# Performance work log

Measured on AMD Instinct MI355X. Metric: run time of the kernel, lower is better.

Reference implementation:

```python
import jax, jax.numpy as jnp
import numpy as np


def setup_inputs() -> dict:
    key = jax.random.key(0)
    kx, ky = jax.random.split(key)
    N, M, D = 16384, 16384, 512
    x = jax.random.normal(kx, (N, D), dtype=jnp.float32)
    y = jax.random.normal(ky, (M, D), dtype=jnp.float32)
    return {"x": x, "y": y, "device": 0}


def reference(x, y, device):
    # torch.cdist(x, y, p=2): pairwise Euclidean distances [N, M]
    # matching torch's large-matrix cdist path), clamped for numerical safety.
    x_sq = jnp.sum(x * x, axis=1, keepdims=True)          # [N, 1]
    y_sq = jnp.sum(y * y, axis=1)                          # [M]
    sq_dists = x_sq + y_sq[None, :] - 2.0 * (x @ y.T)      # [N, M]
    dists = jnp.sqrt(jnp.maximum(sq_dists, 0.0))
    # min over centers (dim=1), then argmax over candidates (dim=0)
    min_dists = jnp.min(dists, axis=1)                     # [N]
    max_id = jnp.argmax(min_dists)
    max_val = min_dists[max_id]
    return max_val, max_id
```

## Files before the change

### kernel.cpp

```cpp
#include <hip/hip_runtime.h>
#include <hip/hip_fp8.h>
#include <math.h>

#define N_ROWS 16384
#define M_ROWS 16384
#define DIM    512
#define JS     8
#define KCAND  256
#define DELTA  0.40f

typedef __attribute__((ext_vector_type(8))) int   int8v;
typedef __attribute__((ext_vector_type(4))) int   int4v;
typedef __attribute__((ext_vector_type(4))) float floatx4;

__global__ __launch_bounds__(256) void convert_kernel(const float* __restrict__ x, const float* __restrict__ y,
                                                      unsigned char* __restrict__ xh8, unsigned char* __restrict__ yh8,
                                                      float* __restrict__ x_sq, float* __restrict__ y_sq,
                                                      unsigned int* __restrict__ gmax_bits,
                                                      unsigned int* __restrict__ cnt, int* __restrict__ cand) {
    if (blockIdx.x == 0) {
        if (threadIdx.x < KCAND) cand[threadIdx.x] = 0;
        if (threadIdx.x == 0) { *gmax_bits = 0u; *cnt = 0u; }
    }
    int wave = threadIdx.x >> 6, lane = threadIdx.x & 63;
    int row = blockIdx.x * 4 + wave;
    const float* src; unsigned char* dst8; float* dsq; int r;
    if (row < N_ROWS) { r = row;          src = x; dst8 = xh8; dsq = x_sq; }
    else              { r = row - N_ROWS; src = y; dst8 = yh8; dsq = y_sq; }
    const float4* s4 = (const float4*)(src + (size_t)r * DIM);
    float4 a = s4[lane * 2];
    float4 b = s4[lane * 2 + 1];
    float v[8] = {a.x, a.y, a.z, a.w, b.x, b.y, b.z, b.w};
    union { unsigned char b[8]; uint2 u2; } pk;
    float s = 0.f;
    #pragma unroll
    for (int i = 0; i < 8; ++i) {
        s += v[i] * v[i];
        __hip_fp8_e4m3 q(v[i]);
        pk.b[i] = (unsigned char)q.__x;
    }
    *(uint2*)(dst8 + (size_t)r * DIM + lane * 8) = pk.u2;
    #pragma unroll
    for (int off = 32; off > 0; off >>= 1) s += __shfl_down(s, off, 64);
    if (lane == 0) dsq[r] = s;
}

__global__ __launch_bounds__(512, 2) void pass1_kernel(const unsigned char* __restrict__ xh8,
                                                       const unsigned char* __restrict__ yh8,
                                                       const float* __restrict__ y_sq,
                                                       float* __restrict__ part) {
    __shared__ __align__(16) unsigned char Bs[4][16384];
    __shared__ __align__(16) float ysq_s[M_ROWS / JS];
    __shared__ float red[4][128];

    const int t = threadIdx.x;
    const int w = t >> 6, lane = t & 63;
    const int col = lane & 15, q = lane >> 4;
    const int h = w >> 2, c = w & 3;

    const int bid = blockIdx.x;
    const int wg = (bid & 7) * 128 + (bid >> 3);
    const int js = wg >> 7;
    const int i0 = (wg & 127) * 128;
    const int jbase = js * (M_ROWS / JS);

    {
        const float4* ys4 = (const float4*)(y_sq + jbase);
        *(float4*)&ysq_s[t * 4] = ys4[t];
    }

    {
        const unsigned char* gs = xh8 + (size_t)i0 * DIM;
        unsigned char* ls = (unsigned char*)Bs;
        #pragma unroll
        for (int it = 0; it < 8; ++it) {
            int s  = it * 512 + t;
            int r  = s >> 5;
            int u  = s & 31;
            int kq = u >> 3;
            int cl = (u & 7) ^ (r & 7);
            __builtin_amdgcn_global_load_lds(
                (const __attribute__((address_space(1))) void*)(gs + r * 512 + kq * 128 + cl * 16),
                (__attribute__((address_space(3))) void*)(ls + it * 8192 + w * 1024),
                16, 0, 0);
        }
    }
    __syncthreads();

    int8v afr[4][4];
    {
        const unsigned char* ab = (const unsigned char*)Bs;
        #pragma unroll
        for (int mt = 0; mt < 4; ++mt) {
            int rr = h * 64 + mt * 16 + col;
            #pragma unroll
            for (int kc = 0; kc < 4; ++kc) {
                int base = rr * 512 + kc * 128 + (((q << 1) ^ (rr & 7)) << 4);
                int4v a0 = *(const int4v*)(ab + base);
                int4v a1 = *(const int4v*)(ab + (base ^ 16));
                int8v f;
                f[0] = a0[0]; f[1] = a0[1]; f[2] = a0[2]; f[3] = a0[3];
                f[4] = a1[0]; f[5] = a1[1]; f[6] = a1[2]; f[7] = a1[3];
                afr[mt][kc] = f;
            }
        }
    }
    __syncthreads();

    int spo[2];
    {
        #pragma unroll
        for (int i = 0; i < 2; ++i) {
            int s  = i * 512 + t;
            int g  = s >> 7, u = s & 127;
            int jl = (g << 4) + (u & 15);
            int c2 = (u >> 4) ^ (u & 7);
            spo[i] = jl * DIM + c2 * 16;
        }
    }
    const unsigned char* tb = yh8 + (size_t)jbase * DIM;
    const int Klane = col * 16 + (((q << 1) ^ (col & 7)) << 8);

    float minv[16];
    #pragma unroll
    for (int i = 0; i < 16; ++i) minv[i] = __builtin_inff();

#define STAGE(BUF, TOFF)                                                                     \
    { _Pragma("unroll")                                                                      \
      for (int i_ = 0; i_ < 2; ++i_) {                                                       \
          __builtin_amdgcn_global_load_lds(                                                  \
              (const __attribute__((address_space(1))) void*)(tb + spo[i_] + (TOFF)),        \
              (__attribute__((address_space(3))) void*)(&Bs[BUF][i_ * 8192 + w * 1024]),     \
              16, 0, 0);                                                                     \
      } }

    STAGE(0, 0)
    STAGE(1, 128)

    for (int jt = 0; jt < 16; ++jt) {
        floatx4 acc[4][2];
        #pragma unroll
        for (int mt = 0; mt < 4; ++mt) {
            acc[mt][0] = (floatx4){0.f, 0.f, 0.f, 0.f};
            acc[mt][1] = (floatx4){0.f, 0.f, 0.f, 0.f};
        }
        #pragma unroll
        for (int kc = 0; kc < 4; ++kc) {
            const int jtp  = (jt + (kc >> 1)) & 15;
            const int toff = jtp * (128 * DIM) + (((kc + 2) & 3) << 7);
            STAGE((kc + 2) & 3, toff)
            asm volatile("s_waitcnt vmcnt(4)" ::: "memory");
            __builtin_amdgcn_s_barrier();
            asm volatile("" ::: "memory");
            #pragma unroll
            for (int nt = 0; nt < 2; ++nt) {
                const unsigned char* gb = &Bs[kc][(c * 2 + nt) * 2048];
                int4v lo = *(const int4v*)(gb + Klane);
                int4v hi = *(const int4v*)(gb + (Klane ^ 256));
                int8v b;
                b[0] = lo[0]; b[1] = lo[1]; b[2] = lo[2]; b[3] = lo[3];
                b[4] = hi[0]; b[5] = hi[1]; b[6] = hi[2]; b[7] = hi[3];
                __builtin_amdgcn_s_setprio(1);
                #pragma unroll
                for (int mt = 0; mt < 4; ++mt)
                    acc[mt][nt] = __builtin_amdgcn_mfma_scale_f32_16x16x128_f8f6f4(
                        afr[mt][kc], b, acc[mt][nt], 0, 0, 0, 127, 0, 127);
                __builtin_amdgcn_s_setprio(0);
            }
        }
        #pragma unroll
        for (int nt = 0; nt < 2; ++nt) {
            float qv = ysq_s[jt * 128 + c * 32 + nt * 16 + col];
            #pragma unroll
            for (int mt = 0; mt < 4; ++mt)
                #pragma unroll
                for (int r = 0; r < 4; ++r)
                    minv[mt * 4 + r] = fminf(minv[mt * 4 + r], qv - 2.f * acc[mt][nt][r]);
        }
    }
#undef STAGE

    #pragma unroll
    for (int i = 0; i < 16; ++i) {
        float v = minv[i];
        v = fminf(v, __shfl_xor(v, 1, 64));
        v = fminf(v, __shfl_xor(v, 2, 64));
        v = fminf(v, __shfl_xor(v, 4, 64));
        v = fminf(v, __shfl_xor(v, 8, 64));
        minv[i] = v;
    }
    if (col == 0) {
        #pragma unroll
        for (int mt = 0; mt < 4; ++mt)
            #pragma unroll
            for (int r = 0; r < 4; ++r)
                red[c][h * 64 + mt * 16 + q * 4 + r] = minv[mt * 4 + r];
    }
    __syncthreads();
    if (t < 128)
        part[(size_t)(i0 + t) * JS + js] =
            fminf(fminf(red[0][t], red[1][t]), fminf(red[2][t], red[3][t]));
}

__global__ __launch_bounds__(1024) void maxred_kernel(const float* __restrict__ part,
                                                      const float* __restrict__ x_sq,
                                                      float* __restrict__ aval,
                                                      unsigned int* __restrict__ gmax_bits) {
    __shared__ float sm[1024];
    int t = threadIdx.x;
    int row = blockIdx.x * 1024 + t;
    float m = part[(size_t)row * JS];
    #pragma unroll
    for (int c = 1; c < JS; ++c) m = fminf(m, part[(size_t)row * JS + c]);
    float v = sqrtf(fmaxf(x_sq[row] + m, 0.f));
    aval[row] = v;
    sm[t] = v;
    __syncthreads();
    for (int s = 512; s > 0; s >>= 1) {
        if (t < s) sm[t] = fmaxf(sm[t], sm[t + s]);
        __syncthreads();
    }
    if (t == 0) atomicMax(gmax_bits, __float_as_uint(sm[0]));
}

__global__ __launch_bounds__(1024) void select_kernel(const float* __restrict__ aval,
                                                      const unsigned int* __restrict__ gmax_bits,
                                                      unsigned int* __restrict__ cnt,
                                                      int* __restrict__ cand) {
    int row = blockIdx.x * 1024 + threadIdx.x;
    float gmax = __uint_as_float(*gmax_bits);
    if (aval[row] >= gmax - DELTA) {
        unsigned s = atomicAdd(cnt, 1u);
        if (s < KCAND) cand[s] = row;
    }
}

#define TIr 64
#define LDA 68
#define LDB 132
__global__ __launch_bounds__(256) void rescore_kernel(const float* __restrict__ x, const float* __restrict__ y,
                                                      const float* __restrict__ y_sq,
                                                      const int* __restrict__ cand,
                                                      const unsigned int* __restrict__ cnt,
                                                      float* __restrict__ part2) {
    __shared__ __align__(16) float As[32 * LDA];
    __shared__ __align__(16) float Bs[32 * LDB];
    __shared__ float red[TIr][17];

    int t = threadIdx.x;
    int tx = t & 15, ty = t >> 4;
    int i0 = blockIdx.x * TIr;
    int j0 = blockIdx.y * 128;

    if ((unsigned)i0 >= *cnt) return;

    float acc[4][8];
    #pragma unroll
    for (int c = 0; c < 4; ++c)
        #pragma unroll
        for (int d = 0; d < 8; ++d) acc[c][d] = 0.f;

    int srow = t >> 3;
    int skq = (t & 7) * 4;
    int grow0 = cand[i0 + srow];
    int grow1 = cand[i0 + 32 + srow];

    for (int kc = 0; kc < DIM; kc += 32) {
        {
            float4 v = *(const float4*)(x + (size_t)grow0 * DIM + kc + skq);
            As[(skq + 0) * LDA + srow] = v.x;
            As[(skq + 1) * LDA + srow] = v.y;
            As[(skq + 2) * LDA + srow] = v.z;
            As[(skq + 3) * LDA + srow] = v.w;
            v = *(const float4*)(x + (size_t)grow1 * DIM + kc + skq);
            As[(skq + 0) * LDA + 32 + srow] = v.x;
            As[(skq + 1) * LDA + 32 + srow] = v.y;
            As[(skq + 2) * LDA + 32 + srow] = v.z;
            As[(skq + 3) * LDA + 32 + srow] = v.w;
        }
        #pragma unroll
        for (int it = 0; it < 4; ++it) {
            int row = it * 32 + srow;
            float4 v = *(const float4*)(y + (size_t)(j0 + row) * DIM + kc + skq);
            Bs[(skq + 0) * LDB + row] = v.x;
            Bs[(skq + 1) * LDB + row] = v.y;
            Bs[(skq + 2) * LDB + row] = v.z;
            Bs[(skq + 3) * LDB + row] = v.w;
        }
        __syncthreads();
        #pragma unroll 8
        for (int k = 0; k < 32; ++k) {
            float4 a  = *(const float4*)&As[k * LDA + ty * 4];
            float4 b0 = *(const float4*)&Bs[k * LDB + tx * 8];
            float4 b1 = *(const float4*)&Bs[k * LDB + tx * 8 + 4];
            float av[4] = {a.x, a.y, a.z, a.w};
            float bv[8] = {b0.x, b0.y, b0.z, b0.w, b1.x, b1.y, b1.z, b1.w};
            #pragma unroll
            for (int c = 0; c < 4; ++c)
                #pragma unroll
                for (int d = 0; d < 8; ++d)
                    acc[c][d] = fmaf(av[c], bv[d], acc[c][d]);
        }
        __syncthreads();
    }

    float4 q0 = *(const float4*)(y_sq + j0 + tx * 8);
    float4 q1 = *(const float4*)(y_sq + j0 + tx * 8 + 4);
    float qv[8] = {q0.x, q0.y, q0.z, q0.w, q1.x, q1.y, q1.z, q1.w};
    float mv[4] = {__builtin_inff(), __builtin_inff(), __builtin_inff(), __builtin_inff()};
    #pragma unroll
    for (int c = 0; c < 4; ++c)
        #pragma unroll
        for (int d = 0; d < 8; ++d)
            mv[c] = fminf(mv[c], qv[d] - 2.f * acc[c][d]);
    #pragma unroll
    for (int c = 0; c < 4; ++c) red[ty * 4 + c][tx] = mv[c];
    __syncthreads();
    if (t < TIr) {
        float m = red[t][0];
        #pragma unroll
        for (int xx = 1; xx < 16; ++xx) m = fminf(m, red[t][xx]);
        part2[(size_t)(i0 + t) * 128 + blockIdx.y] = m;
    }
}

__global__ __launch_bounds__(256) void final2_kernel(const float* __restrict__ part2,
                                                     const float* __restrict__ x_sq,
                                                     const int* __restrict__ cand,
                                                     const unsigned int* __restrict__ cnt,
                                                     float* __restrict__ out) {
    __shared__ float sv[256];
    __shared__ int si[256];
    int t = threadIdx.x;
    const float4* p4 = (const float4*)(part2 + (size_t)t * 128);
    float m = __builtin_inff();
    for (int c = 0; c < 32; ++c) {
        float4 v = p4[c];
        m = fminf(m, fminf(fminf(v.x, v.y), fminf(v.z, v.w)));
    }
    unsigned n = *cnt;
    if (n > KCAND) n = KCAND;
    int row = cand[t];
    float v = (t < (int)n) ? sqrtf(fmaxf(x_sq[row] + m, 0.f)) : -__builtin_inff();
    sv[t] = v; si[t] = row;
    __syncthreads();
    for (int s = 128; s > 0; s >>= 1) {
        if (t < s) {
            float v2 = sv[t + s]; int i2 = si[t + s];
            if (v2 > sv[t] || (v2 == sv[t] && i2 < si[t])) { sv[t] = v2; si[t] = i2; }
        }
        __syncthreads();
    }
    if (t == 0) { out[0] = sv[0]; out[1] = (float)si[0]; }
}

extern "C" void kernel_launch(void* const* d_in, const int* in_sizes, int n_in,
                              void* d_out, int out_size, void* d_ws, size_t ws_size,
                              hipStream_t stream) {
    const float* x = (const float*)d_in[0];
    const float* y = (const float*)d_in[1];
    float* out = (float*)d_out;

    char* w = (char*)d_ws;
    unsigned char* xh8 = (unsigned char*)w;
    unsigned char* yh8 = (unsigned char*)(w + (size_t)8388608);
    float* x_sq = (float*)(w + (size_t)16777216);
    float* y_sq = x_sq + N_ROWS;
    float* part = y_sq + M_ROWS;
    float* aval = part + (size_t)N_ROWS * JS;
    float* part2 = aval + N_ROWS;
    int* cand = (int*)(part2 + KCAND * 128);
    unsigned int* gmax_bits = (unsigned int*)(cand + KCAND);
    unsigned int* cnt = gmax_bits + 1;

    convert_kernel<<<(N_ROWS + M_ROWS) / 4, 256, 0, stream>>>(x, y, xh8, yh8, x_sq, y_sq, gmax_bits, cnt, cand);
    pass1_kernel<<<1024, 512, 0, stream>>>(xh8, yh8, y_sq, part);
    maxred_kernel<<<N_ROWS / 1024, 1024, 0, stream>>>(part, x_sq, aval, gmax_bits);
    select_kernel<<<N_ROWS / 1024, 1024, 0, stream>>>(aval, gmax_bits, cnt, cand);
    dim3 g2(KCAND / TIr, M_ROWS / 128);
    rescore_kernel<<<g2, 256, 0, stream>>>(x, y, y_sq, cand, cnt, part2);
    final2_kernel<<<1, 256, 0, stream>>>(part2, x_sq, cand, cnt, out);
}
```

Before: 285.4 us.

## Give each wave a private LDS ring for B tiles and drop per-step barriers

Shrinks the pass1 block from 8 waves to 4. Each wave now computes a 64x64 output sub-tile (4 N-tiles instead of 2) and streams its own slice of the Y tile into a private LDS region, so the per-k-step workgroup barrier can be removed. Waves then wait only on their own outstanding global-to-LDS loads. LDS use grows to about 128KB per block, which limits occupancy to one block of 4 waves per CU and raises accumulator register pressure.

```diff
diff --git a/kernel.cpp b/kernel.cpp
--- a/kernel.cpp
+++ b/kernel.cpp
@@ -45,18 +45,18 @@
     if (lane == 0) dsq[r] = s;
 }
 
-__global__ __launch_bounds__(512, 2) void pass1_kernel(const unsigned char* __restrict__ xh8,
+__global__ __launch_bounds__(256, 1) void pass1_kernel(const unsigned char* __restrict__ xh8,
                                                        const unsigned char* __restrict__ yh8,
                                                        const float* __restrict__ y_sq,
                                                        float* __restrict__ part) {
-    __shared__ __align__(16) unsigned char Bs[4][16384];
+    __shared__ __align__(16) unsigned char Bs[4][32768];
     __shared__ __align__(16) float ysq_s[M_ROWS / JS];
-    __shared__ float red[4][128];
+    __shared__ float red[2][128];
 
     const int t = threadIdx.x;
     const int w = t >> 6, lane = t & 63;
     const int col = lane & 15, q = lane >> 4;
-    const int h = w >> 2, c = w & 3;
+    const int h = w >> 1, c = w & 1;
 
     const int bid = blockIdx.x;
     const int wg = (bid & 7) * 128 + (bid >> 3);
@@ -66,22 +66,25 @@
 
     {
         const float4* ys4 = (const float4*)(y_sq + jbase);
-        *(float4*)&ysq_s[t * 4] = ys4[t];
+        float4 v0 = ys4[t * 2];
+        float4 v1 = ys4[t * 2 + 1];
+        *(float4*)&ysq_s[t * 8]     = v0;
+        *(float4*)&ysq_s[t * 8 + 4] = v1;
     }
 
     {
         const unsigned char* gs = xh8 + (size_t)i0 * DIM;
         unsigned char* ls = (unsigned char*)Bs;
         #pragma unroll
-        for (int it = 0; it < 8; ++it) {
-            int s  = it * 512 + t;
+        for (int it = 0; it < 16; ++it) {
+            int s  = it * 256 + t;
             int r  = s >> 5;
             int u  = s & 31;
             int kq = u >> 3;
             int cl = (u & 7) ^ (r & 7);
             __builtin_amdgcn_global_load_lds(
                 (const __attribute__((address_space(1))) void*)(gs + r * 512 + kq * 128 + cl * 16),
-                (__attribute__((address_space(3))) void*)(ls + it * 8192 + w * 1024),
+                (__attribute__((address_space(3))) void*)(ls + it * 4096 + w * 1024),
                 16, 0, 0);
         }
     }
@@ -107,18 +110,19 @@
     }
     __syncthreads();
 
-    int spo[2];
+    int spo[8];
     {
         #pragma unroll
-        for (int i = 0; i < 2; ++i) {
-            int s  = i * 512 + t;
+        for (int i = 0; i < 8; ++i) {
+            int s  = i * 64 + lane;
             int g  = s >> 7, u = s & 127;
-            int jl = (g << 4) + (u & 15);
-            int c2 = (u >> 4) ^ (u & 7);
-            spo[i] = jl * DIM + c2 * 16;
+            int jl = c * 64 + (g << 4) + (u & 15);
+            int p  = (u >> 4) ^ (u & 7);
+            spo[i] = jl * DIM + p * 16;
         }
     }
     const unsigned char* tb = yh8 + (size_t)jbase * DIM;
+    unsigned char* mybs = &Bs[w][0];
     const int Klane = col * 16 + (((q << 1) ^ (col & 7)) << 8);
 
     float minv[16];
@@ -127,10 +131,10 @@
 
 #define STAGE(BUF, TOFF)                                                                     \
     { _Pragma("unroll")                                                                      \
-      for (int i_ = 0; i_ < 2; ++i_) {                                                       \
+      for (int i_ = 0; i_ < 8; ++i_) {                                                       \
           __builtin_amdgcn_global_load_lds(                                                  \
               (const __attribute__((address_space(1))) void*)(tb + spo[i_] + (TOFF)),        \
-              (__attribute__((address_space(3))) void*)(&Bs[BUF][i_ * 8192 + w * 1024]),     \
+              (__attribute__((address_space(3))) void*)(mybs + (BUF) * 8192 + i_ * 1024),    \
               16, 0, 0);                                                                     \
       } }
 
@@ -138,23 +142,20 @@
     STAGE(1, 128)
 
     for (int jt = 0; jt < 16; ++jt) {
-        floatx4 acc[4][2];
-        #pragma unroll
-        for (int mt = 0; mt < 4; ++mt) {
-            acc[mt][0] = (floatx4){0.f, 0.f, 0.f, 0.f};
-            acc[mt][1] = (floatx4){0.f, 0.f, 0.f, 0.f};
-        }
+        floatx4 acc[4][4];
+        #pragma unroll
+        for (int mt = 0; mt < 4; ++mt)
+            #pragma unroll
+            for (int nt = 0; nt < 4; ++nt) acc[mt][nt] = (floatx4){0.f, 0.f, 0.f, 0.f};
         #pragma unroll
         for (int kc = 0; kc < 4; ++kc) {
             const int jtp  = (jt + (kc >> 1)) & 15;
             const int toff = jtp * (128 * DIM) + (((kc + 2) & 3) << 7);
             STAGE((kc + 2) & 3, toff)
-            asm volatile("s_waitcnt vmcnt(4)" ::: "memory");
-            __builtin_amdgcn_s_barrier();
-            asm volatile("" ::: "memory");
-            #pragma unroll
-            for (int nt = 0; nt < 2; ++nt) {
-                const unsigned char* gb = &Bs[kc][(c * 2 + nt) * 2048];
+            asm volatile("s_waitcnt vmcnt(16)" ::: "memory");
+            #pragma unroll
+            for (int nt = 0; nt < 4; ++nt) {
+                const unsigned char* gb = mybs + kc * 8192 + nt * 2048;
                 int4v lo = *(const int4v*)(gb + Klane);
                 int4v hi = *(const int4v*)(gb + (Klane ^ 256));
                 int8v b;
@@ -169,8 +170,8 @@
             }
         }
         #pragma unroll
-        for (int nt = 0; nt < 2; ++nt) {
-            float qv = ysq_s[jt * 128 + c * 32 + nt * 16 + col];
+        for (int nt = 0; nt < 4; ++nt) {
+            float qv = ysq_s[jt * 128 + c * 64 + nt * 16 + col];
             #pragma unroll
             for (int mt = 0; mt < 4; ++mt)
                 #pragma unroll
@@ -179,6 +180,8 @@
         }
     }
 #undef STAGE
+
+    asm volatile("s_waitcnt vmcnt(0)" ::: "memory");
 
     #pragma unroll
     for (int i = 0; i < 16; ++i) {
@@ -198,8 +201,7 @@
     }
     __syncthreads();
     if (t < 128)
-        part[(size_t)(i0 + t) * JS + js] =
-            fminf(fminf(red[0][t], red[1][t]), fminf(red[2][t], red[3][t]));
+        part[(size_t)(i0 + t) * JS + js] = fminf(red[0][t], red[1][t]);
 }
 
 __global__ __launch_bounds__(1024) void maxred_kernel(const float* __restrict__ part,
@@ -374,7 +376,7 @@
     unsigned int* cnt = gmax_bits + 1;
 
     convert_kernel<<<(N_ROWS + M_ROWS) / 4, 256, 0, stream>>>(x, y, xh8, yh8, x_sq, y_sq, gmax_bits, cnt, cand);
-    pass1_kernel<<<1024, 512, 0, stream>>>(xh8, yh8, y_sq, part);
+    pass1_kernel<<<1024, 256, 0, stream>>>(xh8, yh8, y_sq, part);
     maxred_kernel<<<N_ROWS / 1024, 1024, 0, stream>>>(part, x_sq, aval, gmax_bits);
     select_kernel<<<N_ROWS / 1024, 1024, 0, stream>>>(aval, gmax_bits, cnt, cand);
     dim3 g2(KCAND / TIr, M_ROWS / 128);
```

Measured after the change: 330.9 us. 1.16x slower.
